# Optimization experiments

Measured on AMD Instinct MI355X. Metric: run time of the kernel, lower is better.

## Reference

```python
import jax, jax.numpy as jnp
import numpy as np

B, L, R, E, D = 16, 28, 64, 34, 512


def setup_inputs() -> dict:
    key = jax.random.key(0)
    ks = jax.random.split(key, 10)
    logits = jax.random.uniform(ks[0], (B, L, R), dtype=jnp.float32)
    evt_embeddings = jax.random.normal(ks[1], (B, 1, D), dtype=jnp.float32)
    arg_embeddings = jax.random.normal(ks[2], (B, L, D), dtype=jnp.float32)
    # valid-arg counts in [1, L] (used as mask-count multiplier and divisor)
    arg_padding_num = jax.random.randint(ks[3], (B,), 1, L + 1).astype(jnp.float32)
    evt_type_list = jax.random.randint(ks[4], (B,), 0, E)
    s = 1.0 / np.sqrt(D)
    WRT = jax.random.normal(ks[5], (R, D, D), dtype=jnp.float32) * s
    WTT = jax.random.normal(ks[6], (E, D, D), dtype=jnp.float32) * s
    w1 = jax.random.normal(ks[7], (D, 64), dtype=jnp.float32) * s
    b1 = jnp.zeros((64,), dtype=jnp.float32)
    w2 = jax.random.normal(ks[8], (64, 1), dtype=jnp.float32) * (1.0 / 8.0)
    b2 = jnp.zeros((1,), dtype=jnp.float32)
    return {"logits": logits, "evt_embeddings": evt_embeddings,
            "arg_embeddings": arg_embeddings, "arg_padding_num": arg_padding_num,
            "evt_type_list": evt_type_list, "WRT": WRT, "WTT": WTT,
            "w1": w1, "b1": b1, "w2": w2, "b2": b2}


def reference(logits, evt_embeddings, arg_embeddings, arg_padding_num,
              evt_type_list, WRT, WTT, w1, b1, w2, b2):
    # role transition matrix per (event, arg): one-hot/soft select over WRT
    # [B,L,R] x [R,D,D] -> [B,L,D,D]  (dominant, memory-bound intermediate)
    role_mats = jnp.einsum('blr,rde->blde', logits, WRT)
    # event transition matrix: one-hot select over WTT == gather
    evt_mats = WTT[evt_type_list]                      # [B,D,D]
    # event embedding transform: [B,1,D] bmm [B,D,D] -> [B,D]
    evt_trans = jnp.einsum('bd,bde->be', evt_embeddings[:, 0, :], evt_mats)
    # per-arg transform: [B,L,D] bmm [B,L,D,D] -> [B,L,D]
    role_trans = jnp.einsum('bld,blde->ble', arg_embeddings, role_mats)
    # multiply by count, sum over args, divide by count (as in the original)
    role_trans = role_trans * arg_padding_num[:, None, None]
    new_sum = jnp.sum(role_trans, axis=1)              # [B,D]
    div = new_sum / arg_padding_num[:, None]
    graph_embeddings = (div + evt_trans) / 2.0         # [B,D]
    # scorer MLP: Linear(D,64) -> ReLU -> Linear(64,1) -> Sigmoid
    h = jax.nn.relu(graph_embeddings @ w1 + b1)
    score = jax.nn.sigmoid(h @ w2 + b2)                # [B,1]
    return score
```

## Files before the change

kernel.cpp:

```cpp
#include <hip/hip_runtime.h>
#include <math.h>

#define BB 16
#define LL 28
#define RR 64
#define DD 512
#define NROLE 512
#define NEVT  256

__global__ void __launch_bounds__(256, 3) kernel_a(
    const float* __restrict__ logits,
    const float* __restrict__ arg,
    const float* __restrict__ WRT,
    const float* __restrict__ WTT,
    const float* __restrict__ evt_emb,
    const int*   __restrict__ evt_type,
    float* __restrict__ part,
    float* __restrict__ evt_part)
{
    __shared__ float smem[1024];
    const int t   = threadIdx.x;
    const int q   = blockIdx.x / 3;
    const int rem = blockIdx.x - 3 * q;

    if (rem == 2) {
        const int cid = q;
        const int b  = cid >> 4;
        const int dc = cid & 15;
        const int d0 = dc * 32;
        const int ty = evt_type[b];
        const float* Wt = WTT + (size_t)ty * DD * DD;
        const int e4 = t & 127;
        const int s  = t >> 7;
        float4 a = {0.f, 0.f, 0.f, 0.f};
#pragma unroll
        for (int db = 0; db < 32; db += 16) {
            float  em[8];
            float4 w[8];
#pragma unroll
            for (int i = 0; i < 8; ++i) {
                const int d = d0 + db + s + 2 * i;
                em[i] = evt_emb[b * DD + d];
                w[i]  = ((const float4*)(Wt + (size_t)d * DD))[e4];
            }
#pragma unroll
            for (int i = 0; i < 8; ++i) {
                a.x = fmaf(em[i], w[i].x, a.x);
                a.y = fmaf(em[i], w[i].y, a.y);
                a.z = fmaf(em[i], w[i].z, a.z);
                a.w = fmaf(em[i], w[i].w, a.w);
            }
        }
        float4* sm4 = (float4*)smem;
        if (s == 1) sm4[e4] = a;
        __syncthreads();
        if (s == 0) {
            const float4 q4 = sm4[e4];
            a.x += q4.x; a.y += q4.y; a.z += q4.z; a.w += q4.w;
            ((float4*)evt_part)[(size_t)cid * 128 + e4] = a;
        }
        return;
    }

    const int rid = 2 * q + rem;
    const int r  = rid >> 3;
    const int d0 = (rid & 7) * 64;

    const float4* Wp = (const float4*)(WRT + ((size_t)r * DD + d0) * DD);

    const int e4 = t & 127;
    const int bh = t >> 7;

    float4 w[8];
#pragma unroll
    for (int i = 0; i < 8; ++i)
        w[i] = Wp[(size_t)i * 128 + e4];

    {
        const int b  = t >> 4;
        const int d4 = t & 15;
        const float4* ap = (const float4*)(arg) + (size_t)(b * LL) * 128 + (d0 >> 2) + d4;
        const float*  lp = logits + (b * LL) * RR + r;
        float4 g = {0.f, 0.f, 0.f, 0.f};
#pragma unroll 7
        for (int l = 0; l < LL; ++l) {
            const float4 av = ap[(size_t)l * 128];
            const float lg = lp[l * RR];
            g.x = fmaf(lg, av.x, g.x);
            g.y = fmaf(lg, av.y, g.y);
            g.z = fmaf(lg, av.z, g.z);
            g.w = fmaf(lg, av.w, g.w);
        }
        smem[(4 * d4 + 0) * 16 + b] = g.x;
        smem[(4 * d4 + 1) * 16 + b] = g.y;
        smem[(4 * d4 + 2) * 16 + b] = g.z;
        smem[(4 * d4 + 3) * 16 + b] = g.w;
    }
    __syncthreads();

    float4 acc[8];
#pragma unroll
    for (int i = 0; i < 8; ++i) acc[i] = make_float4(0.f, 0.f, 0.f, 0.f);

    const float* G = smem;
    for (int kb = 0; kb < 8; ++kb) {
        const int kbn = (kb + 1) & 7;
        float4 wn[8];
#pragma unroll
        for (int i = 0; i < 8; ++i)
            wn[i] = Wp[(size_t)(kbn * 8 + i) * 128 + e4];
#pragma unroll
        for (int i = 0; i < 8; ++i) {
            const int kk = kb * 8 + i;
            const float4 ga = ((const float4*)(G + kk * 16 + 8 * bh))[0];
            const float4 gb = ((const float4*)(G + kk * 16 + 8 * bh))[1];
            acc[0].x = fmaf(ga.x, w[i].x, acc[0].x); acc[0].y = fmaf(ga.x, w[i].y, acc[0].y);
            acc[0].z = fmaf(ga.x, w[i].z, acc[0].z); acc[0].w = fmaf(ga.x, w[i].w, acc[0].w);
            acc[1].x = fmaf(ga.y, w[i].x, acc[1].x); acc[1].y = fmaf(ga.y, w[i].y, acc[1].y);
            acc[1].z = fmaf(ga.y, w[i].z, acc[1].z); acc[1].w = fmaf(ga.y, w[i].w, acc[1].w);
            acc[2].x = fmaf(ga.z, w[i].x, acc[2].x); acc[2].y = fmaf(ga.z, w[i].y, acc[2].y);
            acc[2].z = fmaf(ga.z, w[i].z, acc[2].z); acc[2].w = fmaf(ga.z, w[i].w, acc[2].w);
            acc[3].x = fmaf(ga.w, w[i].x, acc[3].x); acc[3].y = fmaf(ga.w, w[i].y, acc[3].y);
            acc[3].z = fmaf(ga.w, w[i].z, acc[3].z); acc[3].w = fmaf(ga.w, w[i].w, acc[3].w);
            acc[4].x = fmaf(gb.x, w[i].x, acc[4].x); acc[4].y = fmaf(gb.x, w[i].y, acc[4].y);
            acc[4].z = fmaf(gb.x, w[i].z, acc[4].z); acc[4].w = fmaf(gb.x, w[i].w, acc[4].w);
            acc[5].x = fmaf(gb.y, w[i].x, acc[5].x); acc[5].y = fmaf(gb.y, w[i].y, acc[5].y);
            acc[5].z = fmaf(gb.y, w[i].z, acc[5].z); acc[5].w = fmaf(gb.y, w[i].w, acc[5].w);
            acc[6].x = fmaf(gb.z, w[i].x, acc[6].x); acc[6].y = fmaf(gb.z, w[i].y, acc[6].y);
            acc[6].z = fmaf(gb.z, w[i].z, acc[6].z); acc[6].w = fmaf(gb.z, w[i].w, acc[6].w);
            acc[7].x = fmaf(gb.w, w[i].x, acc[7].x); acc[7].y = fmaf(gb.w, w[i].y, acc[7].y);
            acc[7].z = fmaf(gb.w, w[i].z, acc[7].z); acc[7].w = fmaf(gb.w, w[i].w, acc[7].w);
        }
#pragma unroll
        for (int i = 0; i < 8; ++i) w[i] = wn[i];
    }

    float4* po = (float4*)part + (size_t)rid * 2048;
#pragma unroll
    for (int i = 0; i < 8; ++i)
        po[(8 * bh + i) * 128 + e4] = acc[i];
}

__global__ void __launch_bounds__(256) kernel_reduce(
    const float* __restrict__ part,
    const float* __restrict__ evt_part,
    float* __restrict__ div_acc,
    float* __restrict__ evt_acc)
{
    const int t = threadIdx.x;
    if (blockIdx.x < 128) {
        __shared__ float4 sred[256];
        const int oo = t & 15;
        const int pg = t >> 4;
        const int o4 = blockIdx.x * 16 + oo;
        const float4* p4 = (const float4*)part;
        float4 s = {0.f, 0.f, 0.f, 0.f};
#pragma unroll 8
        for (int i = 0; i < 32; ++i) {
            const int p = pg * 32 + i;
            const float4 v = p4[(size_t)p * 2048 + o4];
            s.x += v.x; s.y += v.y; s.z += v.z; s.w += v.w;
        }
        sred[pg * 16 + oo] = s;
        __syncthreads();
        if (t < 16) {
            float4 tot = sred[t];
#pragma unroll
            for (int g = 1; g < 16; ++g) {
                const float4 v = sred[g * 16 + t];
                tot.x += v.x; tot.y += v.y; tot.z += v.z; tot.w += v.w;
            }
            ((float4*)div_acc)[blockIdx.x * 16 + t] = tot;
        }
    } else {
        const int o4 = (blockIdx.x - 128) * 256 + t;
        const int b  = o4 >> 7;
        const int el = o4 & 127;
        const float4* e4p = (const float4*)evt_part;
        float4 s = {0.f, 0.f, 0.f, 0.f};
#pragma unroll
        for (int dc = 0; dc < 16; ++dc) {
            const float4 v = e4p[(size_t)(b * 16 + dc) * 128 + el];
            s.x += v.x; s.y += v.y; s.z += v.z; s.w += v.w;
        }
        ((float4*)evt_acc)[o4] = s;
    }
}

__global__ void __launch_bounds__(256) kernel_mlp(
    const float* __restrict__ div_acc,
    const float* __restrict__ evt_acc,
    const float* __restrict__ w1,
    const float* __restrict__ b1,
    const float* __restrict__ w2,
    const float* __restrict__ b2,
    float* __restrict__ out)
{
    __shared__ float hred[256];
    const int b  = blockIdx.x;
    const int t  = threadIdx.x;
    const int j  = t & 63;
    const int dq = t >> 6;
    float hp = 0.f;
#pragma unroll 8
    for (int i = 0; i < 128; ++i) {
        const int d = dq * 128 + i;
        const float g = (div_acc[b * DD + d] + evt_acc[b * DD + d]) * 0.5f;
        hp = fmaf(g, w1[d * 64 + j], hp);
    }
    hred[t] = hp;
    __syncthreads();
    if (t < 64) {
        float h = b1[j] + hred[j] + hred[64 + j] + hred[128 + j] + hred[192 + j];
        h = fmaxf(h, 0.f);
        float v = h * w2[j];
#pragma unroll
        for (int off = 32; off > 0; off >>= 1) v += __shfl_down(v, off, 64);
        if (j == 0) out[b] = 1.f / (1.f + expf(-(v + b2[0])));
    }
}

extern "C" void kernel_launch(void* const* d_in, const int* in_sizes, int n_in,
                              void* d_out, int out_size, void* d_ws, size_t ws_size,
                              hipStream_t stream) {
    const float* logits   = (const float*)d_in[0];
    const float* evt_emb  = (const float*)d_in[1];
    const float* arg_emb  = (const float*)d_in[2];
    const int*   evt_type = (const int*)d_in[4];
    const float* WRT      = (const float*)d_in[5];
    const float* WTT      = (const float*)d_in[6];
    const float* w1       = (const float*)d_in[7];
    const float* b1       = (const float*)d_in[8];
    const float* w2       = (const float*)d_in[9];
    const float* b2       = (const float*)d_in[10];
    float* out = (float*)d_out;

    float* part     = (float*)d_ws;
    float* evt_part = part + (size_t)NROLE * 8192;
    float* div_acc  = evt_part + NEVT * DD;
    float* evt_acc  = div_acc + BB * DD;

    hipLaunchKernelGGL(kernel_a, dim3(NROLE + NEVT), dim3(256), 0, stream,
                       logits, arg_emb, WRT, WTT, evt_emb, evt_type, part, evt_part);
    hipLaunchKernelGGL(kernel_reduce, dim3(136), dim3(256), 0, stream,
                       part, evt_part, div_acc, evt_acc);
    hipLaunchKernelGGL(kernel_mlp, dim3(BB), dim3(256), 0, stream,
                       div_acc, evt_acc, w1, b1, w2, b2, out);
}
```

Measured before the change: 156.6 us.

## Merge role pairs per block and split K across half-blocks with smem reduction

Each role block now handles two roles (2*rp, 2*rp+1) for a 64-row d chunk, computing 16 batches per thread while the two half-blocks split the K range and combine through shared memory. This halves the number of partial-sum slabs written to global memory and read back by the reduce kernel. The event blocks are no longer interleaved with the role blocks but placed after them. The cost is more accumulator registers, an occupancy hint lowered from 3 to 2, and a larger shared-memory buffer.

```diff
diff --git a/kernel.cpp b/kernel.cpp
--- a/kernel.cpp
+++ b/kernel.cpp
@@ -5,10 +5,10 @@
 #define LL 28
 #define RR 64
 #define DD 512
-#define NROLE 512
+#define NROLE 256
 #define NEVT  256
 
-__global__ void __launch_bounds__(256, 3) kernel_a(
+__global__ void __launch_bounds__(256, 2) kernel_a(
     const float* __restrict__ logits,
     const float* __restrict__ arg,
     const float* __restrict__ WRT,
@@ -18,17 +18,114 @@
     float* __restrict__ part,
     float* __restrict__ evt_part)
 {
-    __shared__ float smem[1024];
+    __shared__ float smem[8192];
     const int t   = threadIdx.x;
-    const int q   = blockIdx.x / 3;
-    const int rem = blockIdx.x - 3 * q;
-
-    if (rem == 2) {
-        const int cid = q;
-        const int b  = cid >> 4;
-        const int dc = cid & 15;
-        const int d0 = dc * 32;
-        const int ty = evt_type[b];
+    const int bid = blockIdx.x;
+
+    if (bid < NROLE) {
+        const int rid = bid;
+        const int rp  = rid >> 3;
+        const int d0  = (rid & 7) * 64;
+
+        const float4* Wp0 = (const float4*)(WRT + ((size_t)(2 * rp)     * DD + d0) * DD);
+        const float4* Wp1 = (const float4*)(WRT + ((size_t)(2 * rp + 1) * DD + d0) * DD);
+
+        const int e4    = t & 127;
+        const int h     = t >> 7;
+        const int kbase = 32 * h;
+
+        float4 w[8];
+#pragma unroll
+        for (int i = 0; i < 8; ++i)
+            w[i] = Wp0[(size_t)(kbase + i) * 128 + e4];
+
+        {
+            const int b  = t >> 4;
+            const int d4 = t & 15;
+            const float4* ap = (const float4*)(arg) + (size_t)(b * LL) * 128 + (d0 >> 2) + d4;
+            const float2* lp = (const float2*)(logits + (size_t)(b * LL) * RR) + rp;
+            float4 g0 = {0.f, 0.f, 0.f, 0.f};
+            float4 g1 = {0.f, 0.f, 0.f, 0.f};
+#pragma unroll 7
+            for (int l = 0; l < LL; ++l) {
+                const float4 av = ap[(size_t)l * 128];
+                const float2 lg = lp[(size_t)l * 32];
+                g0.x = fmaf(lg.x, av.x, g0.x); g0.y = fmaf(lg.x, av.y, g0.y);
+                g0.z = fmaf(lg.x, av.z, g0.z); g0.w = fmaf(lg.x, av.w, g0.w);
+                g1.x = fmaf(lg.y, av.x, g1.x); g1.y = fmaf(lg.y, av.y, g1.y);
+                g1.z = fmaf(lg.y, av.z, g1.z); g1.w = fmaf(lg.y, av.w, g1.w);
+            }
+            smem[(4 * d4 + 0) * 16 + b] = g0.x;
+            smem[(4 * d4 + 1) * 16 + b] = g0.y;
+            smem[(4 * d4 + 2) * 16 + b] = g0.z;
+            smem[(4 * d4 + 3) * 16 + b] = g0.w;
+            smem[1024 + (4 * d4 + 0) * 16 + b] = g1.x;
+            smem[1024 + (4 * d4 + 1) * 16 + b] = g1.y;
+            smem[1024 + (4 * d4 + 2) * 16 + b] = g1.z;
+            smem[1024 + (4 * d4 + 3) * 16 + b] = g1.w;
+        }
+        __syncthreads();
+
+        float4 acc[16];
+#pragma unroll
+        for (int i = 0; i < 16; ++i) acc[i] = make_float4(0.f, 0.f, 0.f, 0.f);
+
+        for (int mb = 0; mb < 8; ++mb) {
+            const int mbn = (mb + 1) & 7;
+            const float4* Wn = (mbn & 4) ? Wp1 : Wp0;
+            const int kn = kbase + (mbn & 3) * 8;
+            float4 wn[8];
+#pragma unroll
+            for (int i = 0; i < 8; ++i)
+                wn[i] = Wn[(size_t)(kn + i) * 128 + e4];
+
+            const float* Gr = smem + (mb & 4) * 256;
+            const int k0 = kbase + (mb & 3) * 8;
+#pragma unroll
+            for (int i = 0; i < 8; ++i) {
+                const float* gp = Gr + (k0 + i) * 16;
+                const float4 ga = ((const float4*)gp)[0];
+                const float4 gb = ((const float4*)gp)[1];
+                const float4 gc = ((const float4*)gp)[2];
+                const float4 gd = ((const float4*)gp)[3];
+#define ACC(j, S) \
+                acc[j].x = fmaf(S, w[i].x, acc[j].x); \
+                acc[j].y = fmaf(S, w[i].y, acc[j].y); \
+                acc[j].z = fmaf(S, w[i].z, acc[j].z); \
+                acc[j].w = fmaf(S, w[i].w, acc[j].w);
+                ACC(0,  ga.x) ACC(1,  ga.y) ACC(2,  ga.z) ACC(3,  ga.w)
+                ACC(4,  gb.x) ACC(5,  gb.y) ACC(6,  gb.z) ACC(7,  gb.w)
+                ACC(8,  gc.x) ACC(9,  gc.y) ACC(10, gc.z) ACC(11, gc.w)
+                ACC(12, gd.x) ACC(13, gd.y) ACC(14, gd.z) ACC(15, gd.w)
+#undef ACC
+            }
+#pragma unroll
+            for (int i = 0; i < 8; ++i) w[i] = wn[i];
+        }
+
+        __syncthreads();
+        float4* cb = (float4*)smem;
+        if (h == 1) {
+#pragma unroll
+            for (int i = 0; i < 16; ++i)
+                cb[i * 128 + e4] = acc[i];
+        }
+        __syncthreads();
+        if (h == 0) {
+            float4* po = (float4*)part + (size_t)rid * 2048;
+#pragma unroll
+            for (int i = 0; i < 16; ++i) {
+                const float4 v = cb[i * 128 + e4];
+                acc[i].x += v.x; acc[i].y += v.y; acc[i].z += v.z; acc[i].w += v.w;
+                po[i * 128 + e4] = acc[i];
+            }
+        }
+    } else {
+        const int cid = bid - NROLE;
+        const int b   = cid >> 4;
+        const int dc  = cid & 15;
+        const int d0  = dc * 32;
+        const int ty  = evt_type[b];
         const float* Wt = WTT + (size_t)ty * DD * DD;
         const int e4 = t & 127;
         const int s  = t >> 7;
@@ -36,19 +133,19 @@
 #pragma unroll
         for (int db = 0; db < 32; db += 16) {
             float  em[8];
-            float4 w[8];
+            float4 wv[8];
 #pragma unroll
             for (int i = 0; i < 8; ++i) {
                 const int d = d0 + db + s + 2 * i;
                 em[i] = evt_emb[b * DD + d];
-                w[i]  = ((const float4*)(Wt + (size_t)d * DD))[e4];
+                wv[i] = ((const float4*)(Wt + (size_t)d * DD))[e4];
             }
 #pragma unroll
             for (int i = 0; i < 8; ++i) {
-                a.x = fmaf(em[i], w[i].x, a.x);
-                a.y = fmaf(em[i], w[i].y, a.y);
-                a.z = fmaf(em[i], w[i].z, a.z);
-                a.w = fmaf(em[i], w[i].w, a.w);
+                a.x = fmaf(em[i], wv[i].x, a.x);
+                a.y = fmaf(em[i], wv[i].y, a.y);
+                a.z = fmaf(em[i], wv[i].z, a.z);
+                a.w = fmaf(em[i], wv[i].w, a.w);
             }
         }
         float4* sm4 = (float4*)smem;
@@ -59,86 +156,7 @@
             a.x += q4.x; a.y += q4.y; a.z += q4.z; a.w += q4.w;
             ((float4*)evt_part)[(size_t)cid * 128 + e4] = a;
         }
-        return;
-    }
-
-    const int rid = 2 * q + rem;
-    const int r  = rid >> 3;
-    const int d0 = (rid & 7) * 64;
-
-    const float4* Wp = (const float4*)(WRT + ((size_t)r * DD + d0) * DD);
-
-    const int e4 = t & 127;
-    const int bh = t >> 7;
-
-    float4 w[8];
-#pragma unroll
-    for (int i = 0; i < 8; ++i)
-        w[i] = Wp[(size_t)i * 128 + e4];
-
-    {
-        const int b  = t >> 4;
-        const int d4 = t & 15;
-        const float4* ap = (const float4*)(arg) + (size_t)(b * LL) * 128 + (d0 >> 2) + d4;
-        const float*  lp = logits + (b * LL) * RR + r;
-        float4 g = {0.f, 0.f, 0.f, 0.f};
-#pragma unroll 7
-        for (int l = 0; l < LL; ++l) {
-            const float4 av = ap[(size_t)l * 128];
-            const float lg = lp[l * RR];
-            g.x = fmaf(lg, av.x, g.x);
-            g.y = fmaf(lg, av.y, g.y);
-            g.z = fmaf(lg, av.z, g.z);
-            g.w = fmaf(lg, av.w, g.w);
-        }
-        smem[(4 * d4 + 0) * 16 + b] = g.x;
-        smem[(4 * d4 + 1) * 16 + b] = g.y;
-        smem[(4 * d4 + 2) * 16 + b] = g.z;
-        smem[(4 * d4 + 3) * 16 + b] = g.w;
-    }
-    __syncthreads();
-
-    float4 acc[8];
-#pragma unroll
-    for (int i = 0; i < 8; ++i) acc[i] = make_float4(0.f, 0.f, 0.f, 0.f);
-
-    const float* G = smem;
-    for (int kb = 0; kb < 8; ++kb) {
-        const int kbn = (kb + 1) & 7;
-        float4 wn[8];
-#pragma unroll
-        for (int i = 0; i < 8; ++i)
-            wn[i] = Wp[(size_t)(kbn * 8 + i) * 128 + e4];
-#pragma unroll
-        for (int i = 0; i < 8; ++i) {
-            const int kk = kb * 8 + i;
-            const float4 ga = ((const float4*)(G + kk * 16 + 8 * bh))[0];
-            const float4 gb = ((const float4*)(G + kk * 16 + 8 * bh))[1];
-            acc[0].x = fmaf(ga.x, w[i].x, acc[0].x); acc[0].y = fmaf(ga.x, w[i].y, acc[0].y);
-            acc[0].z = fmaf(ga.x, w[i].z, acc[0].z); acc[0].w = fmaf(ga.x, w[i].w, acc[0].w);
-            acc[1].x = fmaf(ga.y, w[i].x, acc[1].x); acc[1].y = fmaf(ga.y, w[i].y, acc[1].y);
-            acc[1].z = fmaf(ga.y, w[i].z, acc[1].z); acc[1].w = fmaf(ga.y, w[i].w, acc[1].w);
-            acc[2].x = fmaf(ga.z, w[i].x, acc[2].x); acc[2].y = fmaf(ga.z, w[i].y, acc[2].y);
-            acc[2].z = fmaf(ga.z, w[i].z, acc[2].z); acc[2].w = fmaf(ga.z, w[i].w, acc[2].w);
-            acc[3].x = fmaf(ga.w, w[i].x, acc[3].x); acc[3].y = fmaf(ga.w, w[i].y, acc[3].y);
-            acc[3].z = fmaf(ga.w, w[i].z, acc[3].z); acc[3].w = fmaf(ga.w, w[i].w, acc[3].w);
-            acc[4].x = fmaf(gb.x, w[i].x, acc[4].x); acc[4].y = fmaf(gb.x, w[i].y, acc[4].y);
-            acc[4].z = fmaf(gb.x, w[i].z, acc[4].z); acc[4].w = fmaf(gb.x, w[i].w, acc[4].w);
-            acc[5].x = fmaf(gb.y, w[i].x, acc[5].x); acc[5].y = fmaf(gb.y, w[i].y, acc[5].y);
-            acc[5].z = fmaf(gb.y, w[i].z, acc[5].z); acc[5].w = fmaf(gb.y, w[i].w, acc[5].w);
-            acc[6].x = fmaf(gb.z, w[i].x, acc[6].x); acc[6].y = fmaf(gb.z, w[i].y, acc[6].y);
-            acc[6].z = fmaf(gb.z, w[i].z, acc[6].z); acc[6].w = fmaf(gb.z, w[i].w, acc[6].w);
-            acc[7].x = fmaf(gb.w, w[i].x, acc[7].x); acc[7].y = fmaf(gb.w, w[i].y, acc[7].y);
-            acc[7].z = fmaf(gb.w, w[i].z, acc[7].z); acc[7].w = fmaf(gb.w, w[i].w, acc[7].w);
-        }
-#pragma unroll
-        for (int i = 0; i < 8; ++i) w[i] = wn[i];
-    }
-
-    float4* po = (float4*)part + (size_t)rid * 2048;
-#pragma unroll
-    for (int i = 0; i < 8; ++i)
-        po[(8 * bh + i) * 128 + e4] = acc[i];
+    }
 }
 
 __global__ void __launch_bounds__(256) kernel_reduce(
@@ -156,8 +174,8 @@
         const float4* p4 = (const float4*)part;
         float4 s = {0.f, 0.f, 0.f, 0.f};
 #pragma unroll 8
-        for (int i = 0; i < 32; ++i) {
-            const int p = pg * 32 + i;
+        for (int i = 0; i < 16; ++i) {
+            const int p = pg * 16 + i;
             const float4 v = p4[(size_t)p * 2048 + o4];
             s.x += v.x; s.y += v.y; s.z += v.z; s.w += v.w;
         }
@@ -237,7 +255,7 @@
 
     float* part     = (float*)d_ws;
     float* evt_part = part + (size_t)NROLE * 8192;
-    float* div_acc  = evt_part + NEVT * DD;
+    float* div_acc  = evt_part + (size_t)NEVT * DD;
     float* evt_acc  = div_acc + BB * DD;
 
     hipLaunchKernelGGL(kernel_a, dim3(NROLE + NEVT), dim3(256), 0, stream,
```

Result: faster. 152.1 us (-2.8%).
